# Kernel tuning notes

Measured on AMD Instinct MI355X. Metric: run time of the kernel, lower is better.

## Reference

```python
import jax, jax.numpy as jnp
import numpy as np

B, L, E, H = 4, 2048, 1024, 16
D = E // H
RBF_GAMMA = 0.5


def setup_inputs() -> dict:
    key = jax.random.key(0)
    ks = jax.random.split(key, 8)
    s = 1.0 / np.sqrt(E)  # linear init scale
    return {
        "query": jax.random.normal(ks[0], (B, L, E), jnp.float32),
        "key": jax.random.normal(ks[1], (B, L, E), jnp.float32),
        "value": jax.random.normal(ks[2], (B, L, E), jnp.float32),
        "Wq": jax.random.normal(ks[3], (E, E), jnp.float32) * s,
        "bq": jnp.zeros((E,), jnp.float32),
        "Wk": jax.random.normal(ks[4], (E, E), jnp.float32) * s,
        "bk": jnp.zeros((E,), jnp.float32),
        "Wv": jax.random.normal(ks[5], (E, E), jnp.float32) * s,
        "bv": jnp.zeros((E,), jnp.float32),
        "Wo": jax.random.normal(ks[6], (E, E), jnp.float32) * s,
        "bo": jnp.zeros((E,), jnp.float32),
    }


def _heads(x):
    # (B, L, E) -> (B, H, L, D)
    b, l, _ = x.shape
    return x.reshape(b, l, H, D).transpose(0, 2, 1, 3)


def _rbf_scores(q, k):
    # score[b,h,i,j] = -gamma * ||q_i - k_j||^2   (log of RBF kernel)
    q2 = jnp.sum(q * q, axis=-1)  # (B,H,Lq)
    k2 = jnp.sum(k * k, axis=-1)  # (B,H,Lk)
    qk = jnp.einsum("bhqd,bhkd->bhqk", q, k)  # (B,H,Lq,Lk)
    sqd = q2[..., :, None] + k2[..., None, :] - 2.0 * qk
    return -RBF_GAMMA * sqd


def reference(query, key, value, Wq, bq, Wk, bk, Wv, bv, Wo, bo):
    # Linear projections (torch nn.Linear: x @ W.T + b)
    q = _heads(query @ Wq.T + bq)
    k = _heads(key @ Wk.T + bk)
    v = _heads(value @ Wv.T + bv)
    scores = _rbf_scores(q, k)            # (B,H,L,L)
    attn = jax.nn.softmax(scores, axis=-1)  # dropout p=0.0 (eval)
    out = jnp.einsum("bhqk,bhkd->bhqd", attn, v)
    out = out.transpose(0, 2, 1, 3).reshape(B, L, E)  # merge heads
    return out @ Wo.T + bo
```

## Files before the change

### kernel.cpp

```cpp
#include <hip/hip_runtime.h>
#include <hip/hip_bf16.h>
#include <stdint.h>

#define DEV __device__ __forceinline__

typedef __attribute__((ext_vector_type(8))) __bf16 bf16x8;
typedef __attribute__((ext_vector_type(4))) float f32x4;
typedef __attribute__((ext_vector_type(16))) float f32x16;
typedef __attribute__((ext_vector_type(4))) unsigned int u32x4;

#define LOG2E 1.44269504088896f

DEV unsigned short f2bf(float f) {
    union { float f; unsigned int u; } v; v.f = f;
    unsigned int u = v.u;
    return (unsigned short)((u + 0x7FFFu + ((u >> 16) & 1u)) >> 16);
}
DEV float bf2f(unsigned short s) {
    union { unsigned int u; float f; } v; v.u = ((unsigned int)s) << 16;
    return v.f;
}

DEV f32x4 mfma16(bf16x8 a, bf16x8 b, f32x4 c) {
    return __builtin_amdgcn_mfma_f32_16x16x32_bf16(a, b, c, 0, 0, 0);
}
DEV f32x16 mfma32(bf16x8 a, bf16x8 b, f32x16 c) {
    return __builtin_amdgcn_mfma_f32_32x32x16_bf16(a, b, c, 0, 0, 0);
}
DEV float exp2a(float x) { float r; asm("v_exp_f32 %0, %1" : "=v"(r) : "v"(x)); return r; }
DEV unsigned cvtpk(float lo, float hi) {
    unsigned r; asm("v_cvt_pk_bf16_f32 %0, %1, %2" : "=v"(r) : "v"(lo), "v"(hi)); return r;
}
DEV void plswap(unsigned& x, unsigned& y) {
    asm volatile("v_permlane32_swap_b32 %0, %1" : "+v"(x), "+v"(y));
}

#define GLOAD_LDS16(g, l)                                                          \
    __builtin_amdgcn_global_load_lds((__attribute__((address_space(1))) void*)(g), \
                                     (__attribute__((address_space(3))) void*)(l), \
                                     16, 0, 0)

__global__ void k_cvt_all(const float* __restrict__ i0, const float* __restrict__ i1,
                          const float* __restrict__ i2, const float* __restrict__ i3,
                          const float* __restrict__ i4, const float* __restrict__ i5,
                          const float* __restrict__ i6,
                          unsigned short* __restrict__ o0, unsigned short* __restrict__ o1,
                          unsigned short* __restrict__ o2, unsigned short* __restrict__ o3,
                          unsigned short* __restrict__ o4, unsigned short* __restrict__ o5,
                          unsigned short* __restrict__ o6) {
    int z = blockIdx.y;
    const float* in;
    unsigned short* out;
    int n; float scale = 1.0f;
    switch (z) {
        case 0: in = i0; out = o0; n = 8388608; break;
        case 1: in = i1; out = o1; n = 8388608; break;
        case 2: in = i2; out = o2; n = 8388608; break;
        case 3: in = i3; out = o3; n = 1048576; scale = LOG2E; break;
        case 4: in = i4; out = o4; n = 1048576; break;
        case 5: in = i5; out = o5; n = 1048576; break;
        default: in = i6; out = o6; n = 1048576; break;
    }
    int stride = gridDim.x * blockDim.x;
    for (int i = blockIdx.x * blockDim.x + threadIdx.x; i * 4 < n; i += stride) {
        float4 f = reinterpret_cast<const float4*>(in)[i];
        ushort4 o;
        o.x = f2bf(f.x * scale); o.y = f2bf(f.y * scale);
        o.z = f2bf(f.z * scale); o.w = f2bf(f.w * scale);
        reinterpret_cast<ushort4*>(out)[i] = o;
    }
}

__global__ __launch_bounds__(256) void k_gemm_qkv(
    const unsigned short* __restrict__ xq, const unsigned short* __restrict__ xk,
    const unsigned short* __restrict__ xv, const unsigned short* __restrict__ wq,
    const unsigned short* __restrict__ wk, const unsigned short* __restrict__ wv,
    const float* __restrict__ bq, const float* __restrict__ bk, const float* __restrict__ bv,
    unsigned short* __restrict__ Qb, unsigned short* __restrict__ Kb,
    unsigned short* __restrict__ Vb, float* __restrict__ biask) {
    __shared__ __align__(16) unsigned short As[128 * 64];
    __shared__ __align__(16) unsigned short Bs[128 * 64];
    const int flat = blockIdx.x;
    const int xcd = flat & 7;
    const int bn = (flat >> 3) & 7;
    const int row = xcd * 24 + (flat >> 6);
    const int z = row >> 6;
    const int bm = row & 63;

    const unsigned short* A  = z == 0 ? xq : (z == 1 ? xk : xv);
    const unsigned short* Bw = z == 0 ? wq : (z == 1 ? wk : wv);
    const float* bias = z == 0 ? bq : (z == 1 ? bk : bv);
    const float bscale = z == 0 ? LOG2E : 1.0f;
    const int K = 1024;

    const int tid = threadIdx.x;
    const int lane = tid & 63, w = tid >> 6;
    const int g = lane >> 4, cc = lane & 15;
    const int wm = w >> 1, wn = w & 1;

    f32x4 acc[4][4] = {};
    const int srow = lane >> 3;
    const int scol = (lane & 7) * 8;

    for (int kt = 0; kt < K; kt += 64) {
#pragma unroll
        for (int p = 0; p < 4; ++p) {
            int c = w * 4 + p;
            int rr = c * 8 + srow;
            const unsigned short* gA = A + (size_t)(bm * 128 + rr) * K + kt + scol;
            GLOAD_LDS16(gA, &As[c * 512]);
            const unsigned short* gB = Bw + (size_t)(bn * 128 + rr) * K + kt + scol;
            GLOAD_LDS16(gB, &Bs[c * 512]);
        }
        __syncthreads();
#pragma unroll
        for (int kc = 0; kc < 2; ++kc) {
            bf16x8 af[4], bf[4];
#pragma unroll
            for (int i = 0; i < 4; ++i) {
                af[i] = *reinterpret_cast<const bf16x8*>(&As[(wm * 64 + i * 16 + cc) * 64 + kc * 32 + g * 8]);
                bf[i] = *reinterpret_cast<const bf16x8*>(&Bs[(wn * 64 + i * 16 + cc) * 64 + kc * 32 + g * 8]);
            }
#pragma unroll
            for (int mi = 0; mi < 4; ++mi)
#pragma unroll
                for (int nj = 0; nj < 4; ++nj)
                    acc[mi][nj] = mfma16(af[mi], bf[nj], acc[mi][nj]);
        }
        __syncthreads();
    }

    unsigned short* out = z == 0 ? Qb : (z == 1 ? Kb : Vb);
    float sq[4][4];
#pragma unroll
    for (int mi = 0; mi < 4; ++mi)
#pragma unroll
        for (int r = 0; r < 4; ++r) sq[mi][r] = 0.f;

#pragma unroll
    for (int mi = 0; mi < 4; ++mi) {
#pragma unroll
        for (int nj = 0; nj < 4; ++nj) {
            int n = bn * 128 + wn * 64 + nj * 16 + cc;
            float bvv = bias[n] * bscale;
            int h = n >> 6, d = n & 63;
#pragma unroll
            for (int r = 0; r < 4; ++r) {
                int m = bm * 128 + wm * 64 + mi * 16 + g * 4 + r;
                unsigned short us = f2bf(acc[mi][nj][r] + bvv);
                int b = m >> 11, l = m & 2047;
                out[(((size_t)b * 16 + h) * 2048 + l) * 64 + d] = us;
                if (z == 1) { float vr = bf2f(us); sq[mi][r] += vr * vr; }
            }
        }
    }
    if (z == 1) {
        const int h = bn * 2 + wn;
#pragma unroll
        for (int mi = 0; mi < 4; ++mi)
#pragma unroll
            for (int r = 0; r < 4; ++r) {
                float s = sq[mi][r];
                s += __shfl_xor(s, 1); s += __shfl_xor(s, 2);
                s += __shfl_xor(s, 4); s += __shfl_xor(s, 8);
                if (cc == 0) {
                    int m = bm * 128 + wm * 64 + mi * 16 + g * 4 + r;
                    biask[(((size_t)(m >> 11)) * 16 + h) * 2048 + (m & 2047)] =
                        -0.5f * LOG2E * s;
                }
            }
    }
}

__global__ __launch_bounds__(256) void k_vt(const unsigned short* __restrict__ Vb,
                                            unsigned short* __restrict__ VbT) {
    __shared__ __align__(16) unsigned short T[64 * 72];
    const int blk = blockIdx.x;
    const int bh = blk >> 5, lt = blk & 31;
    const int tid = threadIdx.x;
    const int rr = tid >> 3, seg = tid & 7;
#pragma unroll
    for (int p = 0; p < 2; ++p) {
        int row = p * 32 + rr;
        const unsigned short* src = Vb + ((size_t)bh * 2048 + lt * 64 + row) * 64 + seg * 8;
        *reinterpret_cast<u32x4*>(&T[row * 72 + seg * 8]) = *reinterpret_cast<const u32x4*>(src);
    }
    __syncthreads();
#pragma unroll
    for (int p = 0; p < 2; ++p) {
        int d = p * 32 + rr;
        union { u32x4 v; unsigned short s[8]; } o;
#pragma unroll
        for (int j = 0; j < 8; ++j) o.s[j] = T[(seg * 8 + j) * 72 + d];
        unsigned short* dst = VbT + ((size_t)bh * 64 + d) * 2048 + lt * 64 + seg * 8;
        *reinterpret_cast<u32x4*>(dst) = o.v;
    }
}

__global__ __launch_bounds__(256) void k_gemm_out(const unsigned short* __restrict__ A,
                                                  const unsigned short* __restrict__ Bw,
                                                  const float* __restrict__ bias,
                                                  float* __restrict__ out) {
    __shared__ __align__(16) unsigned short As[128 * 64];
    __shared__ __align__(16) unsigned short Bs[128 * 64];
    const int K = 1024, N = 1024;
    const int flat = blockIdx.x;
    const int xcd = flat & 7;
    const int bn = (flat >> 3) & 7;
    const int bm = xcd * 8 + (flat >> 6);

    const int tid = threadIdx.x;
    const int lane = tid & 63, w = tid >> 6;
    const int g = lane >> 4, cc = lane & 15;
    const int wm = w >> 1, wn = w & 1;

    f32x4 acc[4][4] = {};
    const int srow = lane >> 3;
    const int scol = (lane & 7) * 8;

    for (int kt = 0; kt < K; kt += 64) {
#pragma unroll
        for (int p = 0; p < 4; ++p) {
            int c = w * 4 + p;
            int rr = c * 8 + srow;
            const unsigned short* gA = A + (size_t)(bm * 128 + rr) * K + kt + scol;
            GLOAD_LDS16(gA, &As[c * 512]);
            const unsigned short* gB = Bw + (size_t)(bn * 128 + rr) * K + kt + scol;
            GLOAD_LDS16(gB, &Bs[c * 512]);
        }
        __syncthreads();
#pragma unroll
        for (int kc = 0; kc < 2; ++kc) {
            bf16x8 af[4], bf[4];
#pragma unroll
            for (int i = 0; i < 4; ++i) {
                af[i] = *reinterpret_cast<const bf16x8*>(&As[(wm * 64 + i * 16 + cc) * 64 + kc * 32 + g * 8]);
                bf[i] = *reinterpret_cast<const bf16x8*>(&Bs[(wn * 64 + i * 16 + cc) * 64 + kc * 32 + g * 8]);
            }
#pragma unroll
            for (int mi = 0; mi < 4; ++mi)
#pragma unroll
                for (int nj = 0; nj < 4; ++nj)
                    acc[mi][nj] = mfma16(af[mi], bf[nj], acc[mi][nj]);
        }
        __syncthreads();
    }

#pragma unroll
    for (int mi = 0; mi < 4; ++mi) {
#pragma unroll
        for (int nj = 0; nj < 4; ++nj) {
            int n = bn * 128 + wn * 64 + nj * 16 + cc;
            float bvv = bias[n];
#pragma unroll
            for (int r = 0; r < 4; ++r) {
                int m = bm * 128 + wm * 64 + mi * 16 + g * 4 + r;
                out[(size_t)m * N + n] = acc[mi][nj][r] + bvv;
            }
        }
    }
}

__global__ __launch_bounds__(256, 2) void k_attn5(const unsigned short* __restrict__ Q,
                                                  const unsigned short* __restrict__ K,
                                                  const unsigned short* __restrict__ VT,
                                                  const float* __restrict__ biask,
                                                  unsigned short* __restrict__ Ob) {
    __shared__ __align__(16) unsigned short SM[18432];
    const int tid = threadIdx.x;
    const int lane = tid & 63, w = tid >> 6;
    const int l31 = lane & 31, hi = lane >> 5, l7 = lane & 7;
    const int flat = blockIdx.x;
    const int bh = (flat & 7) * 8 + ((flat >> 3) & 7);
    const int qt = flat >> 6;
    const size_t kvbase = (size_t)bh * 2048 * 64;
    const int q0 = qt * 256 + w * 64;

    bf16x8 qf[2][4];
#pragma unroll
    for (int qb = 0; qb < 2; ++qb)
#pragma unroll
        for (int kc = 0; kc < 4; ++kc)
            qf[qb][kc] = *reinterpret_cast<const bf16x8*>(
                Q + kvbase + (size_t)(q0 + qb * 32 + l31) * 64 + kc * 16 + hi * 8);

    f32x16 ot[2][2] = {};
    float lrun[2] = {0.f, 0.f};
    const int srow = lane >> 3;

    auto stage = [&](int buf, int t) {
        const int kO = buf ? 4096 : 0;
        const int vO = buf ? 12288 : 8192;
#pragma unroll
        for (int i = 0; i < 2; ++i) {
            int r = w * 16 + i * 8 + srow;
            int cb = l7 ^ (r & 7);
            const unsigned short* gk = K + kvbase + (size_t)(t * 64 + r) * 64 + cb * 8;
            GLOAD_LDS16(gk, &SM[kO + (w * 16 + i * 8) * 64]);
            const unsigned short* gv = VT + kvbase + (size_t)r * 2048 + t * 64 + cb * 8;
            GLOAD_LDS16(gv, &SM[vO + (w * 16 + i * 8) * 64]);
        }
        if (w == 0 && lane < 16) {
            const float* gb = biask + bh * 2048 + t * 64 + lane * 4;
            GLOAD_LDS16(gb, &SM[buf ? 16512 : 16384]);
        }
    };

    stage(0, 0);
    int cur = 0;
    for (int t = 0; t < 32; ++t) {
        __syncthreads();
        if (t + 1 < 32) stage(cur ^ 1, t + 1);
        const int kO = cur ? 4096 : 0;
        const int vO = cur ? 12288 : 8192;
        const float* Bl = reinterpret_cast<const float*>(&SM[cur ? 16512 : 16384]);

        f32x4 bb[2][4];
#pragma unroll
        for (int t2 = 0; t2 < 2; ++t2)
#pragma unroll
            for (int g2 = 0; g2 < 4; ++g2)
                bb[t2][g2] = *reinterpret_cast<const f32x4*>(Bl + t2 * 32 + g2 * 8 + hi * 4);

        f32x16 st[2][2];
#pragma unroll
        for (int qb = 0; qb < 2; ++qb)
#pragma unroll
            for (int t2 = 0; t2 < 2; ++t2)
#pragma unroll
                for (int g2 = 0; g2 < 4; ++g2)
#pragma unroll
                    for (int j = 0; j < 4; ++j) st[qb][t2][g2 * 4 + j] = bb[t2][g2][j];

        __builtin_amdgcn_s_setprio(1);
#pragma unroll
        for (int kc = 0; kc < 4; ++kc)
#pragma unroll
            for (int t2 = 0; t2 < 2; ++t2) {
                bf16x8 kf = *reinterpret_cast<const bf16x8*>(
                    &SM[kO + (t2 * 32 + l31) * 64 + ((((kc << 1) | hi) ^ l7) << 3)]);
                st[0][t2] = mfma32(kf, qf[0][kc], st[0][t2]);
                st[1][t2] = mfma32(kf, qf[1][kc], st[1][t2]);
            }
        __builtin_amdgcn_s_setprio(0);

#pragma unroll
        for (int qb = 0; qb < 2; ++qb) {
            float r0 = 0.f, r1 = 0.f;
#pragma unroll
            for (int i = 0; i < 16; ++i) {
                float p0 = exp2a(st[qb][0][i]); st[qb][0][i] = p0; r0 += p0;
                float p1 = exp2a(st[qb][1][i]); st[qb][1][i] = p1; r1 += p1;
            }
            lrun[qb] += r0 + r1;
        }

#pragma unroll
        for (int t2 = 0; t2 < 2; ++t2) {
            bf16x8 fA[2], fB[2];
#pragma unroll
            for (int qb = 0; qb < 2; ++qb) {
                unsigned w0 = cvtpk(st[qb][t2][0], st[qb][t2][1]);
                unsigned w1 = cvtpk(st[qb][t2][2], st[qb][t2][3]);
                unsigned w2 = cvtpk(st[qb][t2][4], st[qb][t2][5]);
                unsigned w3 = cvtpk(st[qb][t2][6], st[qb][t2][7]);
                unsigned w4 = cvtpk(st[qb][t2][8], st[qb][t2][9]);
                unsigned w5 = cvtpk(st[qb][t2][10], st[qb][t2][11]);
                unsigned w6 = cvtpk(st[qb][t2][12], st[qb][t2][13]);
                unsigned w7 = cvtpk(st[qb][t2][14], st[qb][t2][15]);
                plswap(w0, w2); plswap(w1, w3); plswap(w4, w6); plswap(w5, w7);
                u32x4 p0, p1;
                p0[0] = w0; p0[1] = w1; p0[2] = w2; p0[3] = w3;
                p1[0] = w4; p1[1] = w5; p1[2] = w6; p1[3] = w7;
                fA[qb] = __builtin_bit_cast(bf16x8, p0);
                fB[qb] = __builtin_bit_cast(bf16x8, p1);
            }
            const int kb0 = t2 * 2, kb1 = t2 * 2 + 1;
            __builtin_amdgcn_s_setprio(1);
#pragma unroll
            for (int dj = 0; dj < 2; ++dj) {
                bf16x8 v0 = *reinterpret_cast<const bf16x8*>(
                    &SM[vO + (dj * 32 + l31) * 64 + ((((kb0 << 1) | hi) ^ l7) << 3)]);
                bf16x8 v1 = *reinterpret_cast<const bf16x8*>(
                    &SM[vO + (dj * 32 + l31) * 64 + ((((kb1 << 1) | hi) ^ l7) << 3)]);
                ot[0][dj] = mfma32(v0, fA[0], ot[0][dj]);
                ot[0][dj] = mfma32(v1, fB[0], ot[0][dj]);
                ot[1][dj] = mfma32(v0, fA[1], ot[1][dj]);
                ot[1][dj] = mfma32(v1, fB[1], ot[1][dj]);
            }
            __builtin_amdgcn_s_setprio(0);
        }
        cur ^= 1;
    }

    lrun[0] += __shfl_xor(lrun[0], 32);
    lrun[1] += __shfl_xor(lrun[1], 32);

    __syncthreads();
#pragma unroll
    for (int qb = 0; qb < 2; ++qb) {
        float inv = 1.0f / lrun[qb];
        const int base = (w * 64 + qb * 32 + l31) * 72;
#pragma unroll
        for (int dj = 0; dj < 2; ++dj)
#pragma unroll
            for (int i = 0; i < 8; ++i) {
                unsigned pr = cvtpk(ot[qb][dj][2 * i] * inv, ot[qb][dj][2 * i + 1] * inv);
                int d0 = dj * 32 + 2 * (i & 1) + 8 * (i >> 1) + 4 * hi;
                *reinterpret_cast<unsigned*>(&SM[base + d0]) = pr;
            }
    }
    __syncthreads();
    const int b = bh >> 4, h = bh & 15;
#pragma unroll
    for (int pass = 0; pass < 8; ++pass) {
        int row = pass * 32 + (tid >> 3);
        int seg = tid & 7;
        u32x4 vdat = *reinterpret_cast<const u32x4*>(&SM[row * 72 + seg * 8]);
        int l = qt * 256 + row;
        *reinterpret_cast<u32x4*>(Ob + ((size_t)b * 2048 + l) * 1024 + h * 64 + seg * 8) = vdat;
    }
}

extern "C" void kernel_launch(void* const* d_in, const int* in_sizes, int n_in,
                              void* d_out, int out_size, void* d_ws, size_t ws_size,
                              hipStream_t stream) {
    const float* query = (const float*)d_in[0];
    const float* key   = (const float*)d_in[1];
    const float* value = (const float*)d_in[2];
    const float* Wq = (const float*)d_in[3];
    const float* bq = (const float*)d_in[4];
    const float* Wk = (const float*)d_in[5];
    const float* bk = (const float*)d_in[6];
    const float* Wv = (const float*)d_in[7];
    const float* bv = (const float*)d_in[8];
    const float* Wo = (const float*)d_in[9];
    const float* bo = (const float*)d_in[10];

    unsigned short* xq = (unsigned short*)d_ws;
    unsigned short* xk = xq + 8388608;
    unsigned short* xv = xk + 8388608;
    unsigned short* wq = xv + 8388608;
    unsigned short* wk = wq + 1048576;
    unsigned short* wv = wk + 1048576;
    unsigned short* wo = wv + 1048576;
    unsigned short* Qb = wo + 1048576;
    unsigned short* Kb = Qb + 8388608;
    unsigned short* Vb = Kb + 8388608;
    unsigned short* Ob = Vb + 8388608;
    float* biask = (float*)(Ob + 8388608);
    unsigned short* VbT = xv;

    k_cvt_all<<<dim3(1024, 7), 256, 0, stream>>>(query, key, value, Wq, Wk, Wv, Wo,
                                                 xq, xk, xv, wq, wk, wv, wo);

    k_gemm_qkv<<<1536, 256, 0, stream>>>(xq, xk, xv, wq, wk, wv,
                                         bq, bk, bv, Qb, Kb, Vb, biask);

    k_vt<<<2048, 256, 0, stream>>>(Vb, VbT);

    k_attn5<<<512, 256, 0, stream>>>(Qb, Kb, VbT, biask, Ob);

    k_gemm_out<<<512, 256, 0, stream>>>(Ob, wo, bo, (float*)d_out);
}
```

Baseline: 227.4 us.

## Fuse fp32-to-bf16 activation conversion into QKV GEMM A-tile loading

Removes the separate conversion pass over query/key/value; the QKV GEMM now loads fp32 activations into registers, converts to bf16 with packed cvt, and writes them to LDS, prefetching the next k-tile. Only weights are still converted by a smaller kernel. This eliminates a large intermediate write and re-read but doubles the bytes the GEMM fetches per A tile and replaces async direct-to-LDS loads with register staging.

```diff
diff --git a/kernel.cpp b/kernel.cpp
--- a/kernel.cpp
+++ b/kernel.cpp
@@ -40,29 +40,16 @@
                                      (__attribute__((address_space(3))) void*)(l), \
                                      16, 0, 0)
 
-__global__ void k_cvt_all(const float* __restrict__ i0, const float* __restrict__ i1,
-                          const float* __restrict__ i2, const float* __restrict__ i3,
-                          const float* __restrict__ i4, const float* __restrict__ i5,
-                          const float* __restrict__ i6,
-                          unsigned short* __restrict__ o0, unsigned short* __restrict__ o1,
-                          unsigned short* __restrict__ o2, unsigned short* __restrict__ o3,
-                          unsigned short* __restrict__ o4, unsigned short* __restrict__ o5,
-                          unsigned short* __restrict__ o6) {
+__global__ void k_cvtw(const float* __restrict__ i0, const float* __restrict__ i1,
+                       const float* __restrict__ i2, const float* __restrict__ i3,
+                       unsigned short* __restrict__ o0, unsigned short* __restrict__ o1,
+                       unsigned short* __restrict__ o2, unsigned short* __restrict__ o3) {
     int z = blockIdx.y;
-    const float* in;
-    unsigned short* out;
-    int n; float scale = 1.0f;
-    switch (z) {
-        case 0: in = i0; out = o0; n = 8388608; break;
-        case 1: in = i1; out = o1; n = 8388608; break;
-        case 2: in = i2; out = o2; n = 8388608; break;
-        case 3: in = i3; out = o3; n = 1048576; scale = LOG2E; break;
-        case 4: in = i4; out = o4; n = 1048576; break;
-        case 5: in = i5; out = o5; n = 1048576; break;
-        default: in = i6; out = o6; n = 1048576; break;
-    }
+    const float* in = z == 0 ? i0 : (z == 1 ? i1 : (z == 2 ? i2 : i3));
+    unsigned short* out = z == 0 ? o0 : (z == 1 ? o1 : (z == 2 ? o2 : o3));
+    float scale = z == 0 ? LOG2E : 1.0f;
     int stride = gridDim.x * blockDim.x;
-    for (int i = blockIdx.x * blockDim.x + threadIdx.x; i * 4 < n; i += stride) {
+    for (int i = blockIdx.x * blockDim.x + threadIdx.x; i * 4 < 1048576; i += stride) {
         float4 f = reinterpret_cast<const float4*>(in)[i];
         ushort4 o;
         o.x = f2bf(f.x * scale); o.y = f2bf(f.y * scale);
@@ -72,9 +59,9 @@
 }
 
 __global__ __launch_bounds__(256) void k_gemm_qkv(
-    const unsigned short* __restrict__ xq, const unsigned short* __restrict__ xk,
-    const unsigned short* __restrict__ xv, const unsigned short* __restrict__ wq,
-    const unsigned short* __restrict__ wk, const unsigned short* __restrict__ wv,
+    const float* __restrict__ aq, const float* __restrict__ ak, const float* __restrict__ av,
+    const unsigned short* __restrict__ wq, const unsigned short* __restrict__ wk,
+    const unsigned short* __restrict__ wv,
     const float* __restrict__ bq, const float* __restrict__ bk, const float* __restrict__ bv,
     unsigned short* __restrict__ Qb, unsigned short* __restrict__ Kb,
     unsigned short* __restrict__ Vb, float* __restrict__ biask) {
@@ -87,7 +74,7 @@
     const int z = row >> 6;
     const int bm = row & 63;
 
-    const unsigned short* A  = z == 0 ? xq : (z == 1 ? xk : xv);
+    const float* A = z == 0 ? aq : (z == 1 ? ak : av);
     const unsigned short* Bw = z == 0 ? wq : (z == 1 ? wk : wv);
     const float* bias = z == 0 ? bq : (z == 1 ? bk : bv);
     const float bscale = z == 0 ? LOG2E : 1.0f;
@@ -102,17 +89,42 @@
     const int srow = lane >> 3;
     const int scol = (lane & 7) * 8;
 
-    for (int kt = 0; kt < K; kt += 64) {
+    float4 ar[4][2];
+    auto loadA = [&](int kt) {
 #pragma unroll
         for (int p = 0; p < 4; ++p) {
             int c = w * 4 + p;
             int rr = c * 8 + srow;
-            const unsigned short* gA = A + (size_t)(bm * 128 + rr) * K + kt + scol;
-            GLOAD_LDS16(gA, &As[c * 512]);
+            const float* gA = A + (size_t)(bm * 128 + rr) * K + kt + scol;
+            ar[p][0] = *reinterpret_cast<const float4*>(gA);
+            ar[p][1] = *reinterpret_cast<const float4*>(gA + 4);
+        }
+    };
+    auto writeA = [&]() {
+#pragma unroll
+        for (int p = 0; p < 4; ++p) {
+            int c = w * 4 + p;
+            u32x4 pk;
+            pk[0] = cvtpk(ar[p][0].x, ar[p][0].y);
+            pk[1] = cvtpk(ar[p][0].z, ar[p][0].w);
+            pk[2] = cvtpk(ar[p][1].x, ar[p][1].y);
+            pk[3] = cvtpk(ar[p][1].z, ar[p][1].w);
+            *reinterpret_cast<u32x4*>(&As[c * 512 + srow * 64 + scol]) = pk;
+        }
+    };
+
+    loadA(0);
+    for (int kt = 0; kt < K; kt += 64) {
+        writeA();
+#pragma unroll
+        for (int p = 0; p < 4; ++p) {
+            int c = w * 4 + p;
+            int rr = c * 8 + srow;
             const unsigned short* gB = Bw + (size_t)(bn * 128 + rr) * K + kt + scol;
             GLOAD_LDS16(gB, &Bs[c * 512]);
         }
         __syncthreads();
+        if (kt + 64 < K) loadA(kt + 64);
 #pragma unroll
         for (int kc = 0; kc < 2; ++kc) {
             bf16x8 af[4], bf[4];
@@ -437,10 +449,8 @@
     const float* Wo = (const float*)d_in[9];
     const float* bo = (const float*)d_in[10];
 
-    unsigned short* xq = (unsigned short*)d_ws;
-    unsigned short* xk = xq + 8388608;
-    unsigned short* xv = xk + 8388608;
-    unsigned short* wq = xv + 8388608;
+    unsigned short* VbT = (unsigned short*)d_ws;
+    unsigned short* wq = VbT + 8388608;
     unsigned short* wk = wq + 1048576;
     unsigned short* wv = wk + 1048576;
     unsigned short* wo = wv + 1048576;
@@ -449,12 +459,10 @@
     unsigned short* Vb = Kb + 8388608;
     unsigned short* Ob = Vb + 8388608;
     float* biask = (float*)(Ob + 8388608);
-    unsigned short* VbT = xv;
-
-    k_cvt_all<<<dim3(1024, 7), 256, 0, stream>>>(query, key, value, Wq, Wk, Wv, Wo,
-                                                 xq, xk, xv, wq, wk, wv, wo);
-
-    k_gemm_qkv<<<1536, 256, 0, stream>>>(xq, xk, xv, wq, wk, wv,
+
+    k_cvtw<<<dim3(256, 4), 256, 0, stream>>>(Wq, Wk, Wv, Wo, wq, wk, wv, wo);
+
+    k_gemm_qkv<<<1536, 256, 0, stream>>>(query, key, value, wq, wk, wv,
                                          bq, bk, bv, Qb, Kb, Vb, biask);
 
     k_vt<<<2048, 256, 0, stream>>>(Vb, VbT);
```

Result: faster. 215.3 us (-5.3%).
